# Performance work log

Hardware: AMD Instinct MI355X
Metric: run time of the kernel (lower is better)

The kernel has to match this reference:

```python
import jax, jax.numpy as jnp
import numpy as np

DT = 1e-4   # self.dttt
DX = 1.0    # self.dxx
FRE = 100.0 # self.fre
PI = 3.1415926  # constant used literally in the torch code


def setup_inputs() -> dict:
    key = jax.random.key(0)
    k1, k2, k3, k4 = jax.random.split(key, 4)
    H = W = 512
    steps = 256  # coffe * bsize1
    output = jax.random.normal(k1, (steps + 2, 1, H, W), dtype=jnp.float32)
    c = jax.random.uniform(k2, (1, 1, H, W), dtype=jnp.float32)  # wave speed map
    loc_x = jax.random.randint(k3, (3,), 0, 510)
    loc_y = jax.random.randint(k4, (3,), 0, 510)
    return {"output": output, "c": c, "loc_x": loc_x, "loc_y": loc_y,
            "bsize1": 256, "id2": 1, "coffe": 1}


def reference(output, c, loc_x, loc_y, bsize1, id2, coffe):
    # FDTD rollout of get_phy_Loss2. output: [T,1,H,W]; c: [1,1,H,W].
    steps = int(coffe * bsize1)              # number of new frames produced
    cc = c[0, 0]                              # [H, W]
    r = (DT ** 2) * cc ** 2 / (DX ** 2)       # r1 == r2 since dx == dy
    src_mask = loc_x != -1                    # sources with loc_x == -1 are skipped

    def step(carry, n):
        prev, cur = carry                     # frames n-1 and n, each [H, W]
        lap = r[1:-1, 1:-1] * (
            (cur[2:, 1:-1] - 2.0 * cur[1:-1, 1:-1] + cur[:-2, 1:-1])
            + (cur[1:-1, 2:] - 2.0 * cur[1:-1, 1:-1] + cur[1:-1, :-2]))
        interior = 2.0 * cur[1:-1, 1:-1] - prev[1:-1, 1:-1] + lap
        new = jnp.zeros_like(cur).at[1:-1, 1:-1].set(interior)
        # source injection (after interior update, before boundary overwrite)
        src = 1500.0 * jnp.sin(2.0 * PI * FRE * (bsize1 * id2 + n + 1) * DT)
        new = new.at[loc_x, loc_y].set(
            jnp.where(src_mask, src, new[loc_x, loc_y]))
        # absorbing-style boundary updates, applied in the same order as torch:
        new = new.at[0, :].set(cur[0, :] - DT * cc[0, :] * (cur[0, :] - cur[1, :]) / DX)
        new = new.at[:, 0].set(cur[:, 0] - DT * cc[:, 0] * (cur[:, 0] - cur[:, 1]) / DX)
        new = new.at[:, -1].set(cur[:, -1] - DT * cc[:, -1] * (cur[:, -1] - cur[:, -2]) / DX)
        new = new.at[-1, :].set(cur[-1, :] - DT * cc[-1, :] * (cur[-1, :] - cur[-2, :]) / DX)
        return (cur, new), new

    ns = jnp.arange(1, steps + 1)
    _, ys = jax.lax.scan(step, (output[0, 0], output[1, 0]), ns)
    return ys[:, None, :, :]  # [steps, 1, H, W] == output3[2:] unsqueezed
```

## Files before the change

kernel.cpp:

```cpp
#include <hip/hip_runtime.h>


#define HH 512
#define WW 512
#define HW (HH * WW)
#define TILE 32
#define TS 16
#define NW 8
#define RPT 8
#define PHC ((float)(2.0 * 3.1415926 * 100.0))

#define LDS_BARRIER() asm volatile("s_waitcnt lgkmcnt(0)\n\ts_barrier" ::: "memory")

#if __has_builtin(__builtin_amdgcn_update_dpp)
__device__ __forceinline__ float nbrL(float x) {
    int i = __builtin_bit_cast(int, x);
    i = __builtin_amdgcn_update_dpp(i, i, 0x138, 0xf, 0xf, false);
    return __builtin_bit_cast(float, i);
}
__device__ __forceinline__ float nbrR(float x) {
    int i = __builtin_bit_cast(int, x);
    i = __builtin_amdgcn_update_dpp(i, i, 0x130, 0xf, 0xf, false);
    return __builtin_bit_cast(float, i);
}
#else
__device__ __forceinline__ float nbrL(float x) { return __shfl_up(x, 1, 64); }
__device__ __forceinline__ float nbrR(float x) { return __shfl_down(x, 1, 64); }
#endif

__global__ void fdtd_zero_flags(int* f) { f[threadIdx.x] = 0; }

template<bool COLEDGE>
__device__ __forceinline__ void fstep(
    float (&X)[RPT], float (&Y)[RPT],
    const float (&rr)[RPT], const float (&dcv)[RPT],
    const float (*sbR)[2][64], float (*sbW)[2][64],
    int lane, int w, int wup, int sup, int wdn, int sdn,
    bool topw, bool botw, bool isC0, bool isC511,
    bool whs, unsigned smask, const float (&srcT)[260], int n,
    bool keep, float* op)
{
    const float upb = sbR[wup][sup][lane];
    const float dnb = sbR[wdn][sdn][lane];
    #pragma unroll
    for (int j = 0; j < RPT; ++j) {
        const float c = X[j];
        const float u = (j == 0)       ? upb : X[j - 1];
        const float d = (j == RPT - 1) ? dnb : X[j + 1];
        const float lft = nbrL(c);
        const float rgt = nbrR(c);
        Y[j] = 2.f * c - Y[j] + rr[j] * (((u + d) + (lft + rgt)) - 4.f * c);
    }
    if (whs) {
        const float srcv = srcT[n];
        #pragma unroll
        for (int j = 0; j < RPT; ++j)
            if ((smask >> j) & 1u) Y[j] = srcv;
    }
    if (topw) Y[0] = X[0] - dcv[0] * (X[0] - X[1]);
    if (COLEDGE) {
        #pragma unroll
        for (int j = 0; j < RPT; ++j) {
            const float c   = X[j];
            const float rgt = nbrR(c);
            const float lft = nbrL(c);
            float v = Y[j];
            v = isC0   ? (c - dcv[j] * (c - rgt)) : v;
            v = isC511 ? (c - dcv[j] * (c - lft)) : v;
            Y[j] = v;
        }
    }
    if (botw) Y[RPT - 1] = X[RPT - 1] - dcv[RPT - 1] * (X[RPT - 1] - X[RPT - 2]);
    sbW[w][0][lane] = Y[0];
    sbW[w][1][lane] = Y[RPT - 1];
    if (keep) {
        #pragma unroll
        for (int j = 0; j < RPT; ++j)
            __hip_atomic_store(op + j * WW, Y[j], __ATOMIC_RELAXED,
                               __HIP_MEMORY_SCOPE_AGENT);
    }
    LDS_BARRIER();
}

__global__ __launch_bounds__(512)
void fdtd_diet(const float* __restrict__ in_out,
               const float* __restrict__ cmap,
               const int* __restrict__ locx,
               const int* __restrict__ locy,
               const int* __restrict__ pb,
               const int* __restrict__ pid2,
               float* __restrict__ out,
               int steps, int* __restrict__ flags)
{
    __shared__ float sb[2][NW][2][64];
    __shared__ float srcT[260];

    const int tid  = threadIdx.x;
    const int lane = tid & 63;
    const int w    = tid >> 6;
    const int bx   = blockIdx.x & 15;
    const int by   = blockIdx.x >> 4;
    const int gx0  = bx * TILE - TS;
    const int gy0  = by * TILE - TS;
    const int gc   = gx0 + lane;
    const int R    = w * RPT;

    const int lx0 = locx[0], ly0 = locy[0];
    const int lx1 = locx[1], ly1 = locy[1];
    const int lx2 = locx[2], ly2 = locy[2];
    const int Bn  = pb[0] * pid2[0];

    if (tid <= steps && tid < 260)
        srcT[tid] = 1500.0f * __sinf(PHC * (float)(Bn + tid + 1) * 1.0e-4f);

    float A[RPT], B[RPT], rr[RPT], dcv[RPT];
    unsigned smask = 0;
    const bool colOK = (gc >= 0) & (gc < WW);

    #pragma unroll
    for (int j = 0; j < RPT; ++j) {
        const int gr = gy0 + R + j;
        float c = 0.f, ce = 0.f, pp = 0.f;
        if (colOK && gr >= 0 && gr < HH) {
            const int gi = gr * WW + gc;
            c  = cmap[gi];
            ce = in_out[(size_t)HW + gi];
            pp = in_out[gi];
        }
        A[j] = ce; B[j] = pp;
        rr[j]  = 1.0e-8f * c * c;
        dcv[j] = 1.0e-4f * c;
        if ((gr == lx0 && gc == ly0) || (gr == lx1 && gc == ly1) ||
            (gr == lx2 && gc == ly2)) smask |= (1u << j);
    }
    const bool whs     = __any((int)(smask != 0));
    const bool topw    = (by == 0)  && (w == 2);
    const bool botw    = (by == 15) && (w == 5);
    const bool coledge = (bx == 0) || (bx == 15);
    const bool isC0    = (gc == 0);
    const bool isC511  = (gc == WW - 1);
    const bool keep    = (w >= 2) & (w <= 5) & (lane >= 16) & (lane < 48);
    const int  rowOff  = (gy0 + R) * WW + gc;

    const int wup = (w == 0)      ? 0      : w - 1;
    const int sup = (w == 0)      ? 0      : 1;
    const int wdn = (w == NW - 1) ? NW - 1 : w + 1;
    const int sdn = (w == NW - 1) ? 1      : 0;

    sb[0][w][0][lane] = A[0];
    sb[0][w][1][lane] = A[RPT - 1];
    __syncthreads();

    for (int t0 = 0; t0 < steps; t0 += TS) {
        const int nk = (steps - t0 < TS) ? (steps - t0) : TS;

        if (t0 > 0) {
            asm volatile("s_waitcnt vmcnt(0)" ::: "memory");
            __syncthreads();
            if (tid == 0)
                __hip_atomic_store(&flags[blockIdx.x], t0,
                                   __ATOMIC_RELAXED, __HIP_MEMORY_SCOPE_AGENT);
            if (tid < 8) {
                const int dy[8] = {-1,-1,-1, 0, 0, 1, 1, 1};
                const int dx[8] = {-1, 0, 1,-1, 1,-1, 0, 1};
                const int nby = by + dy[tid];
                const int nbx = bx + dx[tid];
                if (nby >= 0 && nby < 16 && nbx >= 0 && nbx < 16) {
                    const int nb = (nby << 4) | nbx;
                    while (__hip_atomic_load(&flags[nb], __ATOMIC_RELAXED,
                                             __HIP_MEMORY_SCOPE_AGENT) < t0)
                        __builtin_amdgcn_s_sleep(2);
                }
            }
            __syncthreads();
            if (!keep) {
                const float* cF = out + (size_t)(t0 - 1) * (size_t)HW;
                const float* pF = cF - HW;
                #pragma unroll
                for (int j = 0; j < RPT; ++j) {
                    const int gr = gy0 + R + j;
                    float ce = 0.f, pp = 0.f;
                    if (colOK && gr >= 0 && gr < HH) {
                        const int gi = gr * WW + gc;
                        ce = __hip_atomic_load(cF + gi, __ATOMIC_RELAXED,
                                               __HIP_MEMORY_SCOPE_AGENT);
                        pp = __hip_atomic_load(pF + gi, __ATOMIC_RELAXED,
                                               __HIP_MEMORY_SCOPE_AGENT);
                    }
                    A[j] = ce; B[j] = pp;
                }
            }
            sb[0][w][0][lane] = A[0];
            sb[0][w][1][lane] = A[RPT - 1];
            __syncthreads();
        }

        float* op = out + (size_t)t0 * (size_t)HW + rowOff;
        if (!coledge) {
            for (int k = 1; k + 1 <= nk; k += 2) {
                fstep<false>(A, B, rr, dcv, sb[0], sb[1], lane, w, wup, sup,
                             wdn, sdn, topw, botw, isC0, isC511, whs, smask,
                             srcT, t0 + k, keep, op);
                op += HW;
                fstep<false>(B, A, rr, dcv, sb[1], sb[0], lane, w, wup, sup,
                             wdn, sdn, topw, botw, isC0, isC511, whs, smask,
                             srcT, t0 + k + 1, keep, op);
                op += HW;
            }
            if (nk & 1) {
                fstep<false>(A, B, rr, dcv, sb[0], sb[1], lane, w, wup, sup,
                             wdn, sdn, topw, botw, isC0, isC511, whs, smask,
                             srcT, t0 + nk, keep, op);
                #pragma unroll
                for (int j = 0; j < RPT; ++j) {
                    const float t = A[j]; A[j] = B[j]; B[j] = t;
                }
            }
        } else {
            for (int k = 1; k + 1 <= nk; k += 2) {
                fstep<true>(A, B, rr, dcv, sb[0], sb[1], lane, w, wup, sup,
                            wdn, sdn, topw, botw, isC0, isC511, whs, smask,
                            srcT, t0 + k, keep, op);
                op += HW;
                fstep<true>(B, A, rr, dcv, sb[1], sb[0], lane, w, wup, sup,
                            wdn, sdn, topw, botw, isC0, isC511, whs, smask,
                            srcT, t0 + k + 1, keep, op);
                op += HW;
            }
            if (nk & 1) {
                fstep<true>(A, B, rr, dcv, sb[0], sb[1], lane, w, wup, sup,
                            wdn, sdn, topw, botw, isC0, isC511, whs, smask,
                            srcT, t0 + nk, keep, op);
                #pragma unroll
                for (int j = 0; j < RPT; ++j) {
                    const float t = A[j]; A[j] = B[j]; B[j] = t;
                }
            }
        }
    }
}

extern "C" void kernel_launch(void* const* d_in, const int* in_sizes, int n_in,
                              void* d_out, int out_size, void* d_ws, size_t ws_size,
                              hipStream_t stream) {
    const float* in_out = (const float*)d_in[0];
    const float* cmap   = (const float*)d_in[1];
    const int*   locx   = (const int*)d_in[2];
    const int*   locy   = (const int*)d_in[3];
    const int*   pb     = (const int*)d_in[4];
    const int*   pid2   = (const int*)d_in[5];
    float*       outp   = (float*)d_out;
    int*         flags  = (int*)d_ws;

    int steps = out_size / HW;

    hipLaunchKernelGGL(fdtd_zero_flags, dim3(1), dim3(256), 0, stream, flags);

    void* args[] = { (void*)&in_out, (void*)&cmap, (void*)&locx, (void*)&locy,
                     (void*)&pb, (void*)&pid2, (void*)&outp, (void*)&steps,
                     (void*)&flags };
    hipLaunchCooperativeKernel((const void*)fdtd_diet,
                               dim3((HH / TILE) * (WW / TILE)),
                               dim3(512), args, 0, stream);
}
```

Before: 215.4 us.

## Shrink vertical halo to 8 rows with 6 rows per wave

Cuts the temporal block from 16 to 8 steps and the vertical halo to 8 rows, so each block covers 48 rows (8 waves × 6 rows) instead of 64 and holds fewer registers per thread. The horizontal halo stays at 16 columns. Stored rows are now picked by a per-wave jlo/jhi range, and the reload step skips only the valid interior region. The aim is less redundant halo computation per step, at the cost of twice as many inter-block flag synchronisations and global reloads.

```diff
diff --git a/kernel.cpp b/kernel.cpp
--- a/kernel.cpp
+++ b/kernel.cpp
@@ -5,9 +5,9 @@
 #define WW 512
 #define HW (HH * WW)
 #define TILE 32
-#define TS 16
+#define TS 8
 #define NW 8
-#define RPT 8
+#define RPT 6
 #define PHC ((float)(2.0 * 3.1415926 * 100.0))
 
 #define LDS_BARRIER() asm volatile("s_waitcnt lgkmcnt(0)\n\ts_barrier" ::: "memory")
@@ -38,7 +38,7 @@
     int lane, int w, int wup, int sup, int wdn, int sdn,
     bool topw, bool botw, bool isC0, bool isC511,
     bool whs, unsigned smask, const float (&srcT)[260], int n,
-    bool keep, float* op)
+    bool lstore, int jlo, int jhi, float* op)
 {
     const float upb = sbR[wup][sup][lane];
     const float dnb = sbR[wdn][sdn][lane];
@@ -57,7 +57,7 @@
         for (int j = 0; j < RPT; ++j)
             if ((smask >> j) & 1u) Y[j] = srcv;
     }
-    if (topw) Y[0] = X[0] - dcv[0] * (X[0] - X[1]);
+    if (topw) Y[2] = X[2] - dcv[2] * (X[2] - X[3]);
     if (COLEDGE) {
         #pragma unroll
         for (int j = 0; j < RPT; ++j) {
@@ -70,12 +70,11 @@
             Y[j] = v;
         }
     }
-    if (botw) Y[RPT - 1] = X[RPT - 1] - dcv[RPT - 1] * (X[RPT - 1] - X[RPT - 2]);
+    if (botw) Y[3] = X[3] - dcv[3] * (X[3] - X[2]);
     sbW[w][0][lane] = Y[0];
     sbW[w][1][lane] = Y[RPT - 1];
-    if (keep) {
-        #pragma unroll
-        for (int j = 0; j < RPT; ++j)
+    if (lstore) {
+        for (int j = jlo; j < jhi; ++j)
             __hip_atomic_store(op + j * WW, Y[j], __ATOMIC_RELAXED,
                                __HIP_MEMORY_SCOPE_AGENT);
     }
@@ -83,14 +82,14 @@
 }
 
 __global__ __launch_bounds__(512)
-void fdtd_diet(const float* __restrict__ in_out,
-               const float* __restrict__ cmap,
-               const int* __restrict__ locx,
-               const int* __restrict__ locy,
-               const int* __restrict__ pb,
-               const int* __restrict__ pid2,
-               float* __restrict__ out,
-               int steps, int* __restrict__ flags)
+void fdtd_ts8(const float* __restrict__ in_out,
+              const float* __restrict__ cmap,
+              const int* __restrict__ locx,
+              const int* __restrict__ locy,
+              const int* __restrict__ pb,
+              const int* __restrict__ pid2,
+              float* __restrict__ out,
+              int steps, int* __restrict__ flags)
 {
     __shared__ float sb[2][NW][2][64];
     __shared__ float srcT[260];
@@ -100,7 +99,7 @@
     const int w    = tid >> 6;
     const int bx   = blockIdx.x & 15;
     const int by   = blockIdx.x >> 4;
-    const int gx0  = bx * TILE - TS;
+    const int gx0  = bx * TILE - 16;
     const int gy0  = by * TILE - TS;
     const int gc   = gx0 + lane;
     const int R    = w * RPT;
@@ -134,12 +133,15 @@
             (gr == lx2 && gc == ly2)) smask |= (1u << j);
     }
     const bool whs     = __any((int)(smask != 0));
-    const bool topw    = (by == 0)  && (w == 2);
-    const bool botw    = (by == 15) && (w == 5);
+    const bool topw    = (by == 0)  && (w == 1);
+    const bool botw    = (by == 15) && (w == 6);
     const bool coledge = (bx == 0) || (bx == 15);
     const bool isC0    = (gc == 0);
     const bool isC511  = (gc == WW - 1);
-    const bool keep    = (w >= 2) & (w <= 5) & (lane >= 16) & (lane < 48);
+    const int  jlo     = max(0, 8 - R);
+    const int  jhi     = min(RPT, 40 - R);
+    const bool lstore  = (lane >= 16) & (lane < 48) & (jlo < jhi);
+    const bool vlane   = (lane >= 8) & (lane < 56);
     const int  rowOff  = (gy0 + R) * WW + gc;
 
     const int wup = (w == 0)      ? 0      : w - 1;
@@ -173,11 +175,12 @@
                 }
             }
             __syncthreads();
-            if (!keep) {
-                const float* cF = out + (size_t)(t0 - 1) * (size_t)HW;
-                const float* pF = cF - HW;
-                #pragma unroll
-                for (int j = 0; j < RPT; ++j) {
+            const float* cF = out + (size_t)(t0 - 1) * (size_t)HW;
+            const float* pF = cF - HW;
+            #pragma unroll
+            for (int j = 0; j < RPT; ++j) {
+                const bool vrow = (R + j >= 8) & (R + j < 40);
+                if (!(vrow & vlane)) {
                     const int gr = gy0 + R + j;
                     float ce = 0.f, pp = 0.f;
                     if (colOK && gr >= 0 && gr < HH) {
@@ -200,17 +203,17 @@
             for (int k = 1; k + 1 <= nk; k += 2) {
                 fstep<false>(A, B, rr, dcv, sb[0], sb[1], lane, w, wup, sup,
                              wdn, sdn, topw, botw, isC0, isC511, whs, smask,
-                             srcT, t0 + k, keep, op);
+                             srcT, t0 + k, lstore, jlo, jhi, op);
                 op += HW;
                 fstep<false>(B, A, rr, dcv, sb[1], sb[0], lane, w, wup, sup,
                              wdn, sdn, topw, botw, isC0, isC511, whs, smask,
-                             srcT, t0 + k + 1, keep, op);
+                             srcT, t0 + k + 1, lstore, jlo, jhi, op);
                 op += HW;
             }
             if (nk & 1) {
                 fstep<false>(A, B, rr, dcv, sb[0], sb[1], lane, w, wup, sup,
                              wdn, sdn, topw, botw, isC0, isC511, whs, smask,
-                             srcT, t0 + nk, keep, op);
+                             srcT, t0 + nk, lstore, jlo, jhi, op);
                 #pragma unroll
                 for (int j = 0; j < RPT; ++j) {
                     const float t = A[j]; A[j] = B[j]; B[j] = t;
@@ -220,17 +223,17 @@
             for (int k = 1; k + 1 <= nk; k += 2) {
                 fstep<true>(A, B, rr, dcv, sb[0], sb[1], lane, w, wup, sup,
                             wdn, sdn, topw, botw, isC0, isC511, whs, smask,
-                            srcT, t0 + k, keep, op);
+                            srcT, t0 + k, lstore, jlo, jhi, op);
                 op += HW;
                 fstep<true>(B, A, rr, dcv, sb[1], sb[0], lane, w, wup, sup,
                             wdn, sdn, topw, botw, isC0, isC511, whs, smask,
-                            srcT, t0 + k + 1, keep, op);
+                            srcT, t0 + k + 1, lstore, jlo, jhi, op);
                 op += HW;
             }
             if (nk & 1) {
                 fstep<true>(A, B, rr, dcv, sb[0], sb[1], lane, w, wup, sup,
                             wdn, sdn, topw, botw, isC0, isC511, whs, smask,
-                            srcT, t0 + nk, keep, op);
+                            srcT, t0 + nk, lstore, jlo, jhi, op);
                 #pragma unroll
                 for (int j = 0; j < RPT; ++j) {
                     const float t = A[j]; A[j] = B[j]; B[j] = t;
@@ -259,7 +262,7 @@
     void* args[] = { (void*)&in_out, (void*)&cmap, (void*)&locx, (void*)&locy,
                      (void*)&pb, (void*)&pid2, (void*)&outp, (void*)&steps,
                      (void*)&flags };
-    hipLaunchCooperativeKernel((const void*)fdtd_diet,
+    hipLaunchCooperativeKernel((const void*)fdtd_ts8,
                                dim3((HH / TILE) * (WW / TILE)),
                                dim3(512), args, 0, stream);
 }
```

Result: slower. 356.6 us (+65.6%).
